# Optimization experiments

Hardware: AMD Instinct MI355X
Metric: run time of the kernel (lower is better)

## Reference

```python
import jax, jax.numpy as jnp
import numpy as np

B, LT, LI, D, H, K = 32, 512, 576, 768, 8, 512


def setup_inputs() -> dict:
    key = jax.random.key(0)
    ks = jax.random.split(key, 10)
    s = 0.02
    return {
        "text_hidden_states": jax.random.normal(ks[0], (B, LT, D), jnp.float32),
        "image_hidden_states": jax.random.normal(ks[1], (B, LI, D), jnp.float32),
        "text_mask": jnp.ones((B, LT), jnp.int32),
        "Wb": jax.random.normal(ks[2], (H, D, D), jnp.float32) * s,   # per-head Linear weights [out,in]
        "Wv": jax.random.normal(ks[3], (K, D), jnp.float32) * s,
        "Wq": jax.random.normal(ks[4], (K, D), jnp.float32) * s,
        "Whv": jax.random.normal(ks[5], (K,), jnp.float32) * s,
        "Whq": jax.random.normal(ks[6], (K,), jnp.float32) * s,
        "Wo": jax.random.normal(ks[7], (D, D * H), jnp.float32) * s,  # output_proj weight [out,in]
        "bo": jnp.zeros((D,), jnp.float32),
    }


def reference(text_hidden_states, image_hidden_states, text_mask, Wb, Wv, Wq, Whv, Whq, Wo, bo):
    text, image = text_hidden_states, image_hidden_states
    # per-head text projection (torch Linear: x @ W.T), batched over heads
    pt = jnp.einsum('bxe,hfe->hbxf', text, Wb)                 # [H,B,LT,D]
    aff = jnp.einsum('hbxe,bye->hbxy', pt, image)              # [H,B,LT,LI]
    wv_v = jnp.einsum('bye,ke->byk', image, Wv)                # [B,LI,K] (head-shared)
    wq_q = jnp.einsum('bxe,ke->bxk', text, Wq)                 # [B,LT,K]
    wqqc = jnp.einsum('bxk,hbxy->hbyk', wq_q, aff)             # [H,B,LI,K]
    wvvc = jnp.einsum('byk,hbxy->hbxk', wv_v, aff)             # [H,B,LT,K]
    h_v = jnp.tanh(wv_v[None] + wqqc)
    h_q = jnp.tanh(wq_q[None] + wvvc)
    att_v = jax.nn.softmax(jnp.einsum('hbyk,k->hby', h_v, Whv), axis=-1)  # over image tokens
    att_q = jax.nn.softmax(jnp.einsum('hbxk,k->hbx', h_q, Whq), axis=-1)  # over text tokens
    ctx_v = jnp.einsum('hby,byd->hbd', att_v, image)
    ctx_q = jnp.einsum('hbx,bxd->hbd', att_q, text)
    head_out = ctx_v + ctx_q                                   # [H,B,D]
    combined = jnp.transpose(head_out, (1, 0, 2)).reshape(text.shape[0], -1)  # [B,H*D]
    return combined @ Wo.T + bo
```

## Files before the change

### kernel.cpp

```cpp
#include <hip/hip_runtime.h>
#include <math.h>

#define B_  32
#define LT_ 512
#define LI_ 576
#define LIP 640
#define D_  768
#define H_  8
#define K_  512
#define NTOK  (LI_ + LT_)
#define CSPLIT 8
#define TPB   (NTOK / CSPLIT)
#define NHEAD ((long)H_ * B_ * D_)

typedef __attribute__((ext_vector_type(4))) short short4v;
typedef __attribute__((ext_vector_type(8))) unsigned short ushort8;
typedef __attribute__((ext_vector_type(8))) _Float16 f16x8;
typedef __attribute__((ext_vector_type(4))) float f32x4;

__device__ __forceinline__ unsigned short f2h(float x) {
  _Float16 h = (_Float16)x;
  return __builtin_bit_cast(unsigned short, h);
}
__device__ __forceinline__ float h2f(unsigned short u) {
  return (float)__builtin_bit_cast(_Float16, u);
}
__device__ __forceinline__ float ftanh(float x) {
  float e = __expf(2.f * x);
  return 1.f - 2.f * __builtin_amdgcn_rcpf(e + 1.f);
}

__device__ __forceinline__ void gl_lds16(const void* g, void* l) {
  __builtin_amdgcn_global_load_lds(
      (const __attribute__((address_space(1))) void*)g,
      (__attribute__((address_space(3))) void*)l, 16, 0, 0);
}

#define EPI_PLAIN 0
#define EPI_T     1
#define EPI_TANH  2
#define EPI_OUT   3

struct Seg {
  const unsigned short *A, *B;
  unsigned short *C, *CT;
  const unsigned short* base;
  const float* wvec;
  float* outv;
  long sA, sB, sC, sCT, sBase;
  int Kd, lda, ldb;
  int gx, gy, nblk, epi, Mlim, valid, ldc, ldt;
};
struct Params { Seg s0, s1, s2; };

__global__ __launch_bounds__(256, 2) void mfma_seg(Params p)
{
  const int orig = blockIdx.x, nwg = gridDim.x;
  const int q8 = nwg >> 3, r8 = nwg & 7;
  const int xcd = orig & 7, idx = orig >> 3;
  const int wg = (xcd < r8 ? xcd * (q8 + 1) : r8 * (q8 + 1) + (xcd - r8) * q8) + idx;

  Seg sg; int local;
  if (wg < p.s0.nblk)                      { sg = p.s0; local = wg; }
  else if (wg < p.s0.nblk + p.s1.nblk)     { sg = p.s1; local = wg - p.s0.nblk; }
  else                                     { sg = p.s2; local = wg - p.s0.nblk - p.s1.nblk; }

  const int bx = local % sg.gx;
  const int tmp2 = local / sg.gx;
  const int by = tmp2 % sg.gy, bz = tmp2 / sg.gy;

  __shared__ unsigned short LDSU[36864];

  const int t = threadIdx.x, lane = t & 63, w = t >> 6;
  const int wr = w >> 1, wc = w & 1;
  const int m0 = bx * 256, n0 = by * 128;
  const int Kd = sg.Kd, lda = sg.lda, ldb = sg.ldb, ldc = sg.ldc;
  const unsigned short* A  = sg.A + (long)bz * sg.sA;
  const unsigned short* Bm = sg.B + (long)bz * sg.sB;

  const int rowb = w * 16 + (lane >> 2);
  const int cswz = ((lane & 3) ^ ((rowb >> 1) & 3)) * 8;
  const bool clampA = (m0 + 256 > sg.Mlim);
  const unsigned short* aSrc = A  + (long)(m0 + rowb) * lda + cswz;
  const unsigned short* bSrc = Bm + (long)(n0 + rowb) * ldb + cswz;
  const int ldsLane = rowb * 32;

  f32x4 acc[8][4];
  #pragma unroll
  for (int i = 0; i < 8; ++i)
    #pragma unroll
    for (int j = 0; j < 4; ++j)
      acc[i][j] = (f32x4){0.f, 0.f, 0.f, 0.f};

  const int rl = lane & 15, g = lane >> 4;
  const int aslot = (g ^ ((rl >> 1) & 3)) << 3;

  auto stage = [&](int bufi, int k0) {
    unsigned short* Ab = LDSU + bufi * 12288;
    unsigned short* Bb = Ab + 8192;
    if (!clampA) {
      #pragma unroll
      for (int q = 0; q < 4; ++q)
        gl_lds16(aSrc + (long)q * 64 * lda + k0, Ab + ldsLane + q * 2048);
    } else {
      #pragma unroll
      for (int q = 0; q < 4; ++q) {
        int rgl = m0 + q * 64 + rowb;
        if (rgl >= sg.Mlim) rgl = sg.Mlim - 1;
        gl_lds16(A + (long)rgl * lda + cswz + k0, Ab + ldsLane + q * 2048);
      }
    }
    #pragma unroll
    for (int q = 0; q < 2; ++q)
      gl_lds16(bSrc + (long)q * 64 * ldb + k0, Bb + ldsLane + q * 2048);
  };

  const int nt = Kd >> 5;
  stage(0, 0);
  if (nt > 1) stage(1, 32);
  if (nt > 2) stage(2, 64);
  int cur = 0;
  for (int tt = 0; tt < nt; ++tt) {
    const int ahead = nt - 1 - tt;
    if (ahead >= 2)      asm volatile("s_waitcnt vmcnt(12)" ::: "memory");
    else if (ahead == 1) asm volatile("s_waitcnt vmcnt(6)"  ::: "memory");
    else                 asm volatile("s_waitcnt vmcnt(0)"  ::: "memory");
    __builtin_amdgcn_s_barrier();
    asm volatile("" ::: "memory");

    const unsigned short* Ab = LDSU + cur * 12288;
    const unsigned short* Bb = Ab + 8192;
    f16x8 af[8], bf[4];
    #pragma unroll
    for (int i = 0; i < 8; ++i)
      af[i] = *(const f16x8*)&Ab[(wr * 128 + i * 16 + rl) * 32 + aslot];
    #pragma unroll
    for (int j = 0; j < 4; ++j)
      bf[j] = *(const f16x8*)&Bb[(wc * 64 + j * 16 + rl) * 32 + aslot];
    __builtin_amdgcn_s_setprio(1);
    #pragma unroll
    for (int i = 0; i < 8; ++i)
      #pragma unroll
      for (int j = 0; j < 4; ++j)
        acc[i][j] = __builtin_amdgcn_mfma_f32_16x16x32_f16(af[i], bf[j], acc[i][j], 0, 0, 0);
    __builtin_amdgcn_s_setprio(0);

    asm volatile("" ::: "memory");
    __builtin_amdgcn_s_barrier();
    if (tt + 3 < nt) stage(cur, (tt + 3) << 5);
    cur = (cur == 2) ? 0 : cur + 1;
  }

  const int rg = lane >> 4;
  if (sg.epi <= EPI_T) {
    unsigned short* C = sg.C + (long)bz * sg.sC;
    #pragma unroll
    for (int i = 0; i < 8; ++i)
      #pragma unroll
      for (int j = 0; j < 4; ++j)
        #pragma unroll
        for (int rr = 0; rr < 4; ++rr) {
          int ml = wr * 128 + i * 16 + rg * 4 + rr;
          int nl = wc * 64 + j * 16 + rl;
          if (m0 + ml < sg.Mlim)
            C[(long)(m0 + ml) * ldc + n0 + nl] = f2h(acc[i][j][rr]);
        }
    if (sg.epi == EPI_T) {
      unsigned short* CT = sg.CT + (long)bz * sg.sCT;
      __syncthreads();
      #pragma unroll
      for (int pp = 0; pp < 2; ++pp) {
        if (wr == pp) {
          #pragma unroll
          for (int i = 0; i < 8; ++i)
            #pragma unroll
            for (int j = 0; j < 4; ++j) {
              int nl = wc * 64 + j * 16 + rl;
              int mh = i * 16 + rg * 4;
              *(short4v*)&LDSU[nl * 136 + mh] = (short4v){
                  (short)f2h(acc[i][j][0]), (short)f2h(acc[i][j][1]),
                  (short)f2h(acc[i][j][2]), (short)f2h(acc[i][j][3])};
            }
        }
        __syncthreads();
        #pragma unroll
        for (int rr = 0; rr < 8; ++rr) {
          int rn = rr * 16 + (t >> 4);
          int m8 = (t & 15) * 8;
          int mg = m0 + pp * 128 + m8;
          if (mg < sg.Mlim)
            *(ushort8*)(CT + (long)(n0 + rn) * sg.ldt + mg) =
                *(const ushort8*)&LDSU[rn * 136 + m8];
        }
        __syncthreads();
      }
    }
  } else if (sg.epi == EPI_TANH) {
    const unsigned short* base = sg.base + (long)bz * sg.sBase;
    float* outp = sg.outv + (long)bz * sg.valid;
    #pragma unroll
    for (int i = 0; i < 8; ++i)
      #pragma unroll
      for (int rr = 0; rr < 4; ++rr) {
        int row = m0 + wr * 128 + i * 16 + rg * 4 + rr;
        if (row < sg.Mlim) {
          float s = 0.f;
          #pragma unroll
          for (int j = 0; j < 4; ++j) {
            int col = n0 + wc * 64 + j * 16 + rl;
            float v = acc[i][j][rr] + h2f(base[(long)row * ldc + col]);
            s += ftanh(v) * sg.wvec[col];
          }
          s += __shfl_xor(s, 1, 64);
          s += __shfl_xor(s, 2, 64);
          s += __shfl_xor(s, 4, 64);
          s += __shfl_xor(s, 8, 64);
          if (rl == 0 && row < sg.valid)
            atomicAdd(&outp[row], s);
        }
      }
  } else {
    float* outp = sg.outv;
    if (wr == 0) {
      #pragma unroll
      for (int i = 0; i < 2; ++i)
        #pragma unroll
        for (int rr = 0; rr < 4; ++rr) {
          int row = i * 16 + rg * 4 + rr;
          #pragma unroll
          for (int j = 0; j < 4; ++j) {
            int col = n0 + wc * 64 + j * 16 + rl;
            atomicAdd(&outp[(long)row * ldc + col], acc[i][j][rr]);
          }
        }
    }
  }
}

struct CSeg { const float* src; unsigned short* dst; long n8; };

__global__ __launch_bounds__(256) void cast_multi(
    CSeg c0, CSeg c1, CSeg c2, CSeg c3, CSeg c4)
{
  long i = (long)blockIdx.x * 256 + threadIdx.x;
  const float* src; unsigned short* dst;
  if      (i < c0.n8)                 { src = c0.src; dst = c0.dst; }
  else if ((i -= c0.n8) < c1.n8)      { src = c1.src; dst = c1.dst; }
  else if ((i -= c1.n8) < c2.n8)      { src = c2.src; dst = c2.dst; }
  else if ((i -= c2.n8) < c3.n8)      { src = c3.src; dst = c3.dst; }
  else if ((i -= c3.n8) < c4.n8)      { src = c4.src; dst = c4.dst; }
  else return;
  float4 v0 = ((const float4*)src)[i * 2];
  float4 v1 = ((const float4*)src)[i * 2 + 1];
  ushort8 o;
  o[0] = f2h(v0.x); o[1] = f2h(v0.y); o[2] = f2h(v0.z); o[3] = f2h(v0.w);
  o[4] = f2h(v1.x); o[5] = f2h(v1.y); o[6] = f2h(v1.z); o[7] = f2h(v1.w);
  *(ushort8*)(dst + i * 8) = o;
}

__global__ __launch_bounds__(256) void cast_pad_image(
    const float* __restrict__ in, unsigned short* __restrict__ out)
{
  long tid = (long)blockIdx.x * 256 + threadIdx.x;
  const long tot = (long)B_ * LIP * (D_ / 8);
  if (tid >= tot) return;
  int e8 = (int)(tid % (D_ / 8));
  long rw = tid / (D_ / 8);
  int y  = (int)(rw % LIP);
  long b = rw / LIP;
  ushort8 o;
  if (y < LI_) {
    const float* p = in + ((b * LI_ + y) * D_ + e8 * 8);
    float4 v0 = *(const float4*)p, v1 = *(const float4*)(p + 4);
    o[0] = f2h(v0.x); o[1] = f2h(v0.y); o[2] = f2h(v0.z); o[3] = f2h(v0.w);
    o[4] = f2h(v1.x); o[5] = f2h(v1.y); o[6] = f2h(v1.z); o[7] = f2h(v1.w);
  } else {
    #pragma unroll
    for (int j = 0; j < 8; ++j) o[j] = 0;
  }
  *(ushort8*)(out + rw * D_ + e8 * 8) = o;
}

__global__ __launch_bounds__(256) void zero_f32(float* __restrict__ p, long n) {
  long i = (long)blockIdx.x * 256 + threadIdx.x;
  if (i < n) p[i] = 0.f;
}

__global__ __launch_bounds__(256) void init_out(
    const float* __restrict__ bo, float* __restrict__ out)
{
  int i = blockIdx.x * 256 + threadIdx.x;
  out[i] = bo[i % D_];
}

__global__ __launch_bounds__(256) void softmax_att(
    const float* __restrict__ lv, const float* __restrict__ lq,
    float* __restrict__ attvG, float* __restrict__ attqG)
{
  const int b = blockIdx.x, h = blockIdx.y;
  const int t = threadIdx.x;
  __shared__ float buf[LI_];
  __shared__ float red[4];

  const float* lvp = lv + ((long)h * B_ + b) * LI_;
  float m = -1e30f;
  for (int i = t; i < LI_; i += 256) m = fmaxf(m, lvp[i]);
  #pragma unroll
  for (int o = 32; o > 0; o >>= 1) m = fmaxf(m, __shfl_down(m, o, 64));
  if ((t & 63) == 0) red[t >> 6] = m;
  __syncthreads();
  m = fmaxf(fmaxf(red[0], red[1]), fmaxf(red[2], red[3]));
  __syncthreads();
  float s = 0.f;
  for (int i = t; i < LI_; i += 256) { float e = __expf(lvp[i] - m); buf[i] = e; s += e; }
  #pragma unroll
  for (int o = 32; o > 0; o >>= 1) s += __shfl_down(s, o, 64);
  if ((t & 63) == 0) red[t >> 6] = s;
  __syncthreads();
  s = red[0] + red[1] + red[2] + red[3];
  {
    float inv = 1.f / s;
    float* op = attvG + ((long)h * B_ + b) * LI_;
    for (int i = t; i < LI_; i += 256) op[i] = buf[i] * inv;
  }
  __syncthreads();

  const float* lqp = lq + ((long)h * B_ + b) * LT_;
  m = -1e30f;
  for (int i = t; i < LT_; i += 256) m = fmaxf(m, lqp[i]);
  #pragma unroll
  for (int o = 32; o > 0; o >>= 1) m = fmaxf(m, __shfl_down(m, o, 64));
  if ((t & 63) == 0) red[t >> 6] = m;
  __syncthreads();
  m = fmaxf(fmaxf(red[0], red[1]), fmaxf(red[2], red[3]));
  __syncthreads();
  s = 0.f;
  for (int i = t; i < LT_; i += 256) { float e = __expf(lqp[i] - m); buf[i] = e; s += e; }
  #pragma unroll
  for (int o = 32; o > 0; o >>= 1) s += __shfl_down(s, o, 64);
  if ((t & 63) == 0) red[t >> 6] = s;
  __syncthreads();
  s = red[0] + red[1] + red[2] + red[3];
  {
    float inv = 1.f / s;
    float* op = attqG + ((long)h * B_ + b) * LT_;
    for (int i = t; i < LT_; i += 256) op[i] = buf[i] * inv;
  }
}

__global__ __launch_bounds__(256) void ctx_part(
    const float* __restrict__ attvG, const float* __restrict__ attqG,
    const unsigned short* __restrict__ text_h,
    float* __restrict__ head_part)
{
  const int b = blockIdx.x, d0 = blockIdx.y * 128, s = blockIdx.z;
  const int t = threadIdx.x, dl = t & 127, g = t >> 7;
  const long IMG_OFF = (long)B_ * LT_ * D_;
  __shared__ float wts[H_][TPB];
  __shared__ long  roff[TPB];
  __shared__ float red[H_][128];
  const int tok0 = s * TPB;
  for (int i = t; i < H_ * TPB; i += 256) {
    int h = i / TPB, j = i % TPB, tok = tok0 + j;
    wts[h][j] = tok < LI_ ? attvG[((long)h * B_ + b) * LI_ + tok]
                          : attqG[((long)h * B_ + b) * LT_ + (tok - LI_)];
  }
  if (t < TPB) {
    int tok = tok0 + t;
    roff[t] = tok < LI_ ? IMG_OFF + ((long)b * LIP + tok) * D_
                        : ((long)b * LT_ + (tok - LI_)) * D_;
  }
  __syncthreads();
  float acc[H_];
  #pragma unroll
  for (int h = 0; h < H_; ++h) acc[h] = 0.f;
  #pragma unroll 4
  for (int j = g; j < TPB; j += 2) {
    float val = h2f(text_h[roff[j] + d0 + dl]);
    #pragma unroll
    for (int h = 0; h < H_; ++h) acc[h] = fmaf(wts[h][j], val, acc[h]);
  }
  if (g == 1) {
    #pragma unroll
    for (int h = 0; h < H_; ++h) red[h][dl] = acc[h];
  }
  __syncthreads();
  if (g == 0) {
    float* hp = head_part + (long)s * NHEAD;
    #pragma unroll
    for (int h = 0; h < H_; ++h)
      hp[((long)h * B_ + b) * D_ + d0 + dl] = acc[h] + red[h][dl];
  }
}

__global__ __launch_bounds__(256) void reduce_head(
    const float* __restrict__ head_part, unsigned short* __restrict__ head16)
{
  long i = (long)blockIdx.x * 256 + threadIdx.x;
  float s = 0.f;
  #pragma unroll
  for (int p = 0; p < CSPLIT; ++p) s += head_part[(long)p * NHEAD + i];
  int d = (int)(i % D_);
  long hb = i / D_;
  int b = (int)(hb % B_), h = (int)(hb / B_);
  head16[(long)b * (H_ * D_) + (long)h * D_ + d] = f2h(s);
}

extern "C" void kernel_launch(void* const* d_in, const int* in_sizes, int n_in,
                              void* d_out, int out_size, void* d_ws, size_t ws_size,
                              hipStream_t stream)
{
  const float* text  = (const float*)d_in[0];
  const float* image = (const float*)d_in[1];
  const float* Wb  = (const float*)d_in[3];
  const float* Wv  = (const float*)d_in[4];
  const float* Wq  = (const float*)d_in[5];
  const float* Whv = (const float*)d_in[6];
  const float* Whq = (const float*)d_in[7];
  const float* Wo  = (const float*)d_in[8];
  const float* bo  = (const float*)d_in[9];
  float* out = (float*)d_out;

  const long N_TEXT = (long)B_ * LT_ * D_;
  const long N_IMGP = (long)B_ * LIP * D_;
  const long N_WV   = (long)K_ * D_;
  const long N_WB   = (long)H_ * D_ * D_;
  const long N_WO   = (long)D_ * H_ * D_;
  const long N_WVV  = (long)B_ * LIP * K_;
  const long N_WQQ  = (long)B_ * LT_ * K_;
  const long N_PT   = (long)B_ * LT_ * D_;
  const long N_AFF  = (long)B_ * LT_ * LIP;
  const long N_LV   = (long)H_ * B_ * LI_;
  const long N_LQ   = (long)H_ * B_ * LT_;
  const long N_H16  = (long)B_ * H_ * D_;

  unsigned short* wsu = (unsigned short*)d_ws;
  long off = 0;
  unsigned short* text_h  = wsu + off; off += N_TEXT;
  unsigned short* image_p = wsu + off; off += N_IMGP;
  unsigned short* Wv_h    = wsu + off; off += N_WV;
  unsigned short* Wq_h    = wsu + off; off += N_WV;
  unsigned short* Wb_h    = wsu + off; off += N_WB;
  unsigned short* Wo_h    = wsu + off; off += N_WO;
  unsigned short* wv_v    = wsu + off; off += N_WVV;
  unsigned short* wq_q    = wsu + off; off += N_WQQ;
  unsigned short* wv_vT   = wsu + off; off += N_WVV;
  unsigned short* wq_qT   = wsu + off; off += N_WQQ;
  unsigned short* pt_h    = wsu + off; off += N_PT;
  unsigned short* aff     = wsu + off; off += N_AFF;
  unsigned short* affT    = wsu + off; off += N_AFF;
  unsigned short* head16  = wsu + off; off += N_H16;
  float* lv        = (float*)(wsu + off);
  float* lq        = lv + N_LV;
  float* attvG     = lq + N_LQ;
  float* attqG     = attvG + N_LV;
  float* head_part = attqG + N_LQ;
  const size_t need = (size_t)off * 2 +
      (size_t)(2 * (N_LV + N_LQ) + CSPLIT * NHEAD) * 4;
  if (ws_size < need) return;

  dim3 blk(256);

  {
    CSeg c0{text, text_h, N_TEXT / 8};
    CSeg c1{Wv,   Wv_h,   N_WV / 8};
    CSeg c2{Wq,   Wq_h,   N_WV / 8};
    CSeg c3{Wb,   Wb_h,   N_WB / 8};
    CSeg c4{Wo,   Wo_h,   N_WO / 8};
    long tot8 = c0.n8 + c1.n8 + c2.n8 + c3.n8 + c4.n8;
    cast_multi<<<(unsigned)((tot8 + 255) / 256), blk, 0, stream>>>(c0, c1, c2, c3, c4);
  }
  cast_pad_image<<<(unsigned)((B_ * LIP * (D_ / 8) + 255) / 256), blk, 0, stream>>>(image, image_p);
  zero_f32<<<(unsigned)((N_LV + N_LQ + 255) / 256), blk, 0, stream>>>(lv, N_LV + N_LQ);
  init_out<<<(unsigned)(B_ * D_ / 256), blk, 0, stream>>>(bo, out);

  Seg zs{};  zs.nblk = 0;

  {
    Seg s0{}; s0.A = image_p; s0.B = Wv_h; s0.C = wv_v; s0.CT = wv_vT;
    s0.sA = (long)LIP * D_; s0.sC = (long)LIP * K_; s0.sCT = (long)K_ * LIP;
    s0.Kd = D_; s0.lda = D_; s0.ldb = D_;
    s0.gx = 3; s0.gy = 4; s0.nblk = 3 * 4 * B_; s0.epi = EPI_T;
    s0.Mlim = LIP; s0.ldc = K_; s0.ldt = LIP;

    Seg s1{}; s1.A = text_h; s1.B = Wq_h; s1.C = wq_q; s1.CT = wq_qT;
    s1.sA = (long)LT_ * D_; s1.sC = (long)LT_ * K_; s1.sCT = (long)K_ * LT_;
    s1.Kd = D_; s1.lda = D_; s1.ldb = D_;
    s1.gx = 2; s1.gy = 4; s1.nblk = 2 * 4 * B_; s1.epi = EPI_T;
    s1.Mlim = LT_; s1.ldc = K_; s1.ldt = LT_;

    Seg s2{}; s2.A = text_h; s2.B = Wb_h; s2.C = pt_h;
    s2.Kd = D_; s2.lda = D_; s2.ldb = D_;
    s2.gx = 64; s2.gy = 6; s2.nblk = 64 * 6; s2.epi = EPI_PLAIN;
    s2.Mlim = B_ * LT_; s2.ldc = D_;

    Params P{s0, s1, s2};
    mfma_seg<<<s0.nblk + s1.nblk + s2.nblk, blk, 0, stream>>>(P);
  }

  for (int h = 0; h < H_; ++h) {
    {
      Seg s0{}; s0.A = pt_h; s0.B = image_p; s0.C = aff; s0.CT = affT;
      s0.sA = (long)LT_ * D_; s0.sB = (long)LIP * D_;
      s0.sC = (long)LT_ * LIP; s0.sCT = (long)LIP * LT_;
      s0.Kd = D_; s0.lda = D_; s0.ldb = D_;
      s0.gx = 2; s0.gy = 5; s0.nblk = 2 * 5 * B_; s0.epi = EPI_T;
      s0.Mlim = LT_; s0.ldc = LIP; s0.ldt = LT_;
      Params P{s0, zs, zs};
      mfma_seg<<<s0.nblk, blk, 0, stream>>>(P);
    }
    {
      Seg s0{}; s0.A = affT; s0.B = wq_qT;
      s0.base = wv_v; s0.wvec = Whv; s0.outv = lv + (long)h * B_ * LI_;
      s0.sA = (long)LIP * LT_; s0.sB = (long)K_ * LT_; s0.sBase = (long)LIP * K_;
      s0.Kd = LT_; s0.lda = LT_; s0.ldb = LT_;
      s0.gx = 3; s0.gy = 4; s0.nblk = 3 * 4 * B_; s0.epi = EPI_TANH;
      s0.Mlim = LIP; s0.valid = LI_; s0.ldc = K_;

      Seg s1{}; s1.A = aff; s1.B = wv_vT;
      s1.base = wq_q; s1.wvec = Whq; s1.outv = lq + (long)h * B_ * LT_;
      s1.sA = (long)LT_ * LIP; s1.sB = (long)K_ * LIP; s1.sBase = (long)LT_ * K_;
      s1.Kd = LIP; s1.lda = LIP; s1.ldb = LIP;
      s1.gx = 2; s1.gy = 4; s1.nblk = 2 * 4 * B_; s1.epi = EPI_TANH;
      s1.Mlim = LT_; s1.valid = LT_; s1.ldc = K_;

      Seg s2 = zs;
      if (h < H_ - 1) {
        s2.A = text_h; s2.B = Wb_h + (long)(h + 1) * D_ * D_; s2.C = pt_h;
        s2.Kd = D_; s2.lda = D_; s2.ldb = D_;
        s2.gx = 64; s2.gy = 6; s2.nblk = 64 * 6; s2.epi = EPI_PLAIN;
        s2.Mlim = B_ * LT_; s2.ldc = D_;
      }
      Params P{s0, s1, s2};
      mfma_seg<<<s0.nblk + s1.nblk + s2.nblk, blk, 0, stream>>>(P);
    }
  }

  softmax_att<<<dim3(B_, H_), blk, 0, stream>>>(lv, lq, attvG, attqG);
  ctx_part<<<dim3(B_, D_ / 128, CSPLIT), blk, 0, stream>>>(attvG, attqG, text_h, head_part);
  reduce_head<<<(unsigned)(NHEAD / 256), blk, 0, stream>>>(head_part, head16);

  {
    Seg s0{}; s0.A = head16; s0.B = Wo_h; s0.outv = out;
    s0.sA = (long)(H_ * D_ / 8); s0.sB = (long)(H_ * D_ / 8);
    s0.Kd = H_ * D_ / 8; s0.lda = H_ * D_; s0.ldb = H_ * D_;
    s0.gx = 1; s0.gy = 6; s0.nblk = 1 * 6 * 8; s0.epi = EPI_OUT;
    s0.Mlim = B_; s0.valid = B_; s0.ldc = D_;
    Params P{s0, zs, zs};
    mfma_seg<<<s0.nblk, blk, 0, stream>>>(P);
  }
}
```

Before: 1.068 ms.

## Shrink MFMA GEMM tile to 128x128 for higher occupancy and more blocks

Cuts the per-block M tile from 256 to 128 rows, which reduces accumulator registers and LDS. Launch bounds rise to three blocks per CU and the grid sizes are doubled to match. LDS fragment loads now use explicit ds_read_b128 with a waitcnt and a sched barrier ahead of the MFMAs. The transpose epilogue is simplified into a single pass. In exchange, each block reuses less data per K step, so more global and LDS traffic is needed per flop.

```diff
diff --git a/kernel.cpp b/kernel.cpp
--- a/kernel.cpp
+++ b/kernel.cpp
@@ -36,6 +36,14 @@
       (__attribute__((address_space(3))) void*)l, 16, 0, 0);
 }
 
+__device__ __forceinline__ f16x8 lds_read16(const unsigned short* p) {
+  f16x8 r;
+  const __attribute__((address_space(3))) unsigned short* lp =
+      (const __attribute__((address_space(3))) unsigned short*)p;
+  asm volatile("ds_read_b128 %0, %1" : "=v"(r) : "v"(lp));
+  return r;
+}
+
 #define EPI_PLAIN 0
 #define EPI_T     1
 #define EPI_TANH  2
@@ -53,7 +61,7 @@
 };
 struct Params { Seg s0, s1, s2; };
 
-__global__ __launch_bounds__(256, 2) void mfma_seg(Params p)
+__global__ __launch_bounds__(256, 3) void mfma_seg(Params p)
 {
   const int orig = blockIdx.x, nwg = gridDim.x;
   const int q8 = nwg >> 3, r8 = nwg & 7;
@@ -69,25 +77,25 @@
   const int tmp2 = local / sg.gx;
   const int by = tmp2 % sg.gy, bz = tmp2 / sg.gy;
 
-  __shared__ unsigned short LDSU[36864];
+  __shared__ unsigned short LDSU[24576];
 
   const int t = threadIdx.x, lane = t & 63, w = t >> 6;
   const int wr = w >> 1, wc = w & 1;
-  const int m0 = bx * 256, n0 = by * 128;
+  const int m0 = bx * 128, n0 = by * 128;
   const int Kd = sg.Kd, lda = sg.lda, ldb = sg.ldb, ldc = sg.ldc;
   const unsigned short* A  = sg.A + (long)bz * sg.sA;
   const unsigned short* Bm = sg.B + (long)bz * sg.sB;
 
-  const int rowb = w * 16 + (lane >> 2);
-  const int cswz = ((lane & 3) ^ ((rowb >> 1) & 3)) * 8;
-  const bool clampA = (m0 + 256 > sg.Mlim);
-  const unsigned short* aSrc = A  + (long)(m0 + rowb) * lda + cswz;
-  const unsigned short* bSrc = Bm + (long)(n0 + rowb) * ldb + cswz;
-  const int ldsLane = rowb * 32;
-
-  f32x4 acc[8][4];
-  #pragma unroll
-  for (int i = 0; i < 8; ++i)
+  const int srow = w * 16 + (lane >> 2);
+  const int cswz = ((lane & 3) ^ ((srow >> 1) & 3)) * 8;
+  const bool clampA = (m0 + 128 > sg.Mlim);
+  const unsigned short* aSrc = A  + (long)(m0 + srow) * lda + cswz;
+  const unsigned short* bSrc = Bm + (long)(n0 + srow) * ldb + cswz;
+  const int ldsLane = w * 512 + lane * 8;
+
+  f32x4 acc[4][4];
+  #pragma unroll
+  for (int i = 0; i < 4; ++i)
     #pragma unroll
     for (int j = 0; j < 4; ++j)
       acc[i][j] = (f32x4){0.f, 0.f, 0.f, 0.f};
@@ -96,23 +104,20 @@
   const int aslot = (g ^ ((rl >> 1) & 3)) << 3;
 
   auto stage = [&](int bufi, int k0) {
-    unsigned short* Ab = LDSU + bufi * 12288;
-    unsigned short* Bb = Ab + 8192;
+    unsigned short* Ab = LDSU + bufi * 8192;
+    unsigned short* Bb = Ab + 4096;
     if (!clampA) {
-      #pragma unroll
-      for (int q = 0; q < 4; ++q)
-        gl_lds16(aSrc + (long)q * 64 * lda + k0, Ab + ldsLane + q * 2048);
+      gl_lds16(aSrc + k0,                 Ab + ldsLane);
+      gl_lds16(aSrc + (long)64 * lda + k0, Ab + ldsLane + 2048);
     } else {
-      #pragma unroll
-      for (int q = 0; q < 4; ++q) {
-        int rgl = m0 + q * 64 + rowb;
-        if (rgl >= sg.Mlim) rgl = sg.Mlim - 1;
-        gl_lds16(A + (long)rgl * lda + cswz + k0, Ab + ldsLane + q * 2048);
-      }
+      int r0 = m0 + srow, r1 = r0 + 64;
+      if (r0 >= sg.Mlim) r0 = sg.Mlim - 1;
+      if (r1 >= sg.Mlim) r1 = sg.Mlim - 1;
+      gl_lds16(A + (long)r0 * lda + cswz + k0, Ab + ldsLane);
+      gl_lds16(A + (long)r1 * lda + cswz + k0, Ab + ldsLane + 2048);
     }
-    #pragma unroll
-    for (int q = 0; q < 2; ++q)
-      gl_lds16(bSrc + (long)q * 64 * ldb + k0, Bb + ldsLane + q * 2048);
+    gl_lds16(bSrc + k0,                 Bb + ldsLane);
+    gl_lds16(bSrc + (long)64 * ldb + k0, Bb + ldsLane + 2048);
   };
 
   const int nt = Kd >> 5;
@@ -122,30 +127,31 @@
   int cur = 0;
   for (int tt = 0; tt < nt; ++tt) {
     const int ahead = nt - 1 - tt;
-    if (ahead >= 2)      asm volatile("s_waitcnt vmcnt(12)" ::: "memory");
-    else if (ahead == 1) asm volatile("s_waitcnt vmcnt(6)"  ::: "memory");
-    else                 asm volatile("s_waitcnt vmcnt(0)"  ::: "memory");
+    if (ahead >= 2)      asm volatile("s_waitcnt vmcnt(8)" ::: "memory");
+    else if (ahead == 1) asm volatile("s_waitcnt vmcnt(4)" ::: "memory");
+    else                 asm volatile("s_waitcnt vmcnt(0)" ::: "memory");
     __builtin_amdgcn_s_barrier();
-    asm volatile("" ::: "memory");
-
-    const unsigned short* Ab = LDSU + cur * 12288;
-    const unsigned short* Bb = Ab + 8192;
-    f16x8 af[8], bf[4];
-    #pragma unroll
-    for (int i = 0; i < 8; ++i)
-      af[i] = *(const f16x8*)&Ab[(wr * 128 + i * 16 + rl) * 32 + aslot];
+
+    const unsigned short* Ab = LDSU + cur * 8192;
+    const unsigned short* Bb = Ab + 4096;
+    f16x8 af[4], bf[4];
+    #pragma unroll
+    for (int i = 0; i < 4; ++i)
+      af[i] = lds_read16(&Ab[(wr * 64 + i * 16 + rl) * 32 + aslot]);
     #pragma unroll
     for (int j = 0; j < 4; ++j)
-      bf[j] = *(const f16x8*)&Bb[(wc * 64 + j * 16 + rl) * 32 + aslot];
+      bf[j] = lds_read16(&Bb[(wc * 64 + j * 16 + rl) * 32 + aslot]);
+    asm volatile("s_waitcnt lgkmcnt(0)" ::: "memory");
+    __builtin_amdgcn_sched_barrier(0);
+
     __builtin_amdgcn_s_setprio(1);
     #pragma unroll
-    for (int i = 0; i < 8; ++i)
+    for (int i = 0; i < 4; ++i)
       #pragma unroll
       for (int j = 0; j < 4; ++j)
         acc[i][j] = __builtin_amdgcn_mfma_f32_16x16x32_f16(af[i], bf[j], acc[i][j], 0, 0, 0);
     __builtin_amdgcn_s_setprio(0);
 
-    asm volatile("" ::: "memory");
     __builtin_amdgcn_s_barrier();
     if (tt + 3 < nt) stage(cur, (tt + 3) << 5);
     cur = (cur == 2) ? 0 : cur + 1;
@@ -154,55 +160,49 @@
   const int rg = lane >> 4;
   if (sg.epi <= EPI_T) {
     unsigned short* C = sg.C + (long)bz * sg.sC;
-    #pragma unroll
-    for (int i = 0; i < 8; ++i)
+    unsigned short hv[4][4][4];
+    #pragma unroll
+    for (int i = 0; i < 4; ++i)
       #pragma unroll
       for (int j = 0; j < 4; ++j)
         #pragma unroll
         for (int rr = 0; rr < 4; ++rr) {
-          int ml = wr * 128 + i * 16 + rg * 4 + rr;
+          int ml = wr * 64 + i * 16 + rg * 4 + rr;
           int nl = wc * 64 + j * 16 + rl;
+          hv[i][j][rr] = f2h(acc[i][j][rr]);
           if (m0 + ml < sg.Mlim)
-            C[(long)(m0 + ml) * ldc + n0 + nl] = f2h(acc[i][j][rr]);
+            C[(long)(m0 + ml) * ldc + n0 + nl] = hv[i][j][rr];
         }
     if (sg.epi == EPI_T) {
       unsigned short* CT = sg.CT + (long)bz * sg.sCT;
+      #pragma unroll
+      for (int i = 0; i < 4; ++i)
+        #pragma unroll
+        for (int j = 0; j < 4; ++j) {
+          int nl = wc * 64 + j * 16 + rl;
+          int mh = wr * 64 + i * 16 + rg * 4;
+          *(short4v*)&LDSU[nl * 136 + mh] = (short4v){
+              (short)hv[i][j][0], (short)hv[i][j][1],
+              (short)hv[i][j][2], (short)hv[i][j][3]};
+        }
       __syncthreads();
       #pragma unroll
-      for (int pp = 0; pp < 2; ++pp) {
-        if (wr == pp) {
-          #pragma unroll
-          for (int i = 0; i < 8; ++i)
-            #pragma unroll
-            for (int j = 0; j < 4; ++j) {
-              int nl = wc * 64 + j * 16 + rl;
-              int mh = i * 16 + rg * 4;
-              *(short4v*)&LDSU[nl * 136 + mh] = (short4v){
-                  (short)f2h(acc[i][j][0]), (short)f2h(acc[i][j][1]),
-                  (short)f2h(acc[i][j][2]), (short)f2h(acc[i][j][3])};
-            }
-        }
-        __syncthreads();
-        #pragma unroll
-        for (int rr = 0; rr < 8; ++rr) {
-          int rn = rr * 16 + (t >> 4);
-          int m8 = (t & 15) * 8;
-          int mg = m0 + pp * 128 + m8;
-          if (mg < sg.Mlim)
-            *(ushort8*)(CT + (long)(n0 + rn) * sg.ldt + mg) =
-                *(const ushort8*)&LDSU[rn * 136 + m8];
-        }
-        __syncthreads();
+      for (int rr = 0; rr < 8; ++rr) {
+        int rn = rr * 16 + (t >> 4);
+        int m8 = (t & 15) * 8;
+        if (m0 + m8 < sg.Mlim)
+          *(ushort8*)(CT + (long)(n0 + rn) * sg.ldt + m0 + m8) =
+              *(const ushort8*)&LDSU[rn * 136 + m8];
       }
     }
   } else if (sg.epi == EPI_TANH) {
     const unsigned short* base = sg.base + (long)bz * sg.sBase;
     float* outp = sg.outv + (long)bz * sg.valid;
     #pragma unroll
-    for (int i = 0; i < 8; ++i)
+    for (int i = 0; i < 4; ++i)
       #pragma unroll
       for (int rr = 0; rr < 4; ++rr) {
-        int row = m0 + wr * 128 + i * 16 + rg * 4 + rr;
+        int row = m0 + wr * 64 + i * 16 + rg * 4 + rr;
         if (row < sg.Mlim) {
           float s = 0.f;
           #pragma unroll
@@ -480,18 +480,18 @@
     Seg s0{}; s0.A = image_p; s0.B = Wv_h; s0.C = wv_v; s0.CT = wv_vT;
     s0.sA = (long)LIP * D_; s0.sC = (long)LIP * K_; s0.sCT = (long)K_ * LIP;
     s0.Kd = D_; s0.lda = D_; s0.ldb = D_;
-    s0.gx = 3; s0.gy = 4; s0.nblk = 3 * 4 * B_; s0.epi = EPI_T;
+    s0.gx = 5; s0.gy = 4; s0.nblk = 5 * 4 * B_; s0.epi = EPI_T;
     s0.Mlim = LIP; s0.ldc = K_; s0.ldt = LIP;
 
     Seg s1{}; s1.A = text_h; s1.B = Wq_h; s1.C = wq_q; s1.CT = wq_qT;
     s1.sA = (long)LT_ * D_; s1.sC = (long)LT_ * K_; s1.sCT = (long)K_ * LT_;
     s1.Kd = D_; s1.lda = D_; s1.ldb = D_;
-    s1.gx = 2; s1.gy = 4; s1.nblk = 2 * 4 * B_; s1.epi = EPI_T;
+    s1.gx = 4; s1.gy = 4; s1.nblk = 4 * 4 * B_; s1.epi = EPI_T;
     s1.Mlim = LT_; s1.ldc = K_; s1.ldt = LT_;
 
     Seg s2{}; s2.A = text_h; s2.B = Wb_h; s2.C = pt_h;
     s2.Kd = D_; s2.lda = D_; s2.ldb = D_;
-    s2.gx = 64; s2.gy = 6; s2.nblk = 64 * 6; s2.epi = EPI_PLAIN;
+    s2.gx = 128; s2.gy = 6; s2.nblk = 128 * 6; s2.epi = EPI_PLAIN;
     s2.Mlim = B_ * LT_; s2.ldc = D_;
 
     Params P{s0, s1, s2};
@@ -504,7 +504,7 @@
       s0.sA = (long)LT_ * D_; s0.sB = (long)LIP * D_;
       s0.sC = (long)LT_ * LIP; s0.sCT = (long)LIP * LT_;
       s0.Kd = D_; s0.lda = D_; s0.ldb = D_;
-      s0.gx = 2; s0.gy = 5; s0.nblk = 2 * 5 * B_; s0.epi = EPI_T;
+      s0.gx = 4; s0.gy = 5; s0.nblk = 4 * 5 * B_; s0.epi = EPI_T;
       s0.Mlim = LT_; s0.ldc = LIP; s0.ldt = LT_;
       Params P{s0, zs, zs};
       mfma_seg<<<s0.nblk, blk, 0, stream>>>(P);
@@ -514,21 +514,21 @@
       s0.base = wv_v; s0.wvec = Whv; s0.outv = lv + (long)h * B_ * LI_;
       s0.sA = (long)LIP * LT_; s0.sB = (long)K_ * LT_; s0.sBase = (long)LIP * K_;
       s0.Kd = LT_; s0.lda = LT_; s0.ldb = LT_;
-      s0.gx = 3; s0.gy = 4; s0.nblk = 3 * 4 * B_; s0.epi = EPI_TANH;
+      s0.gx = 5; s0.gy = 4; s0.nblk = 5 * 4 * B_; s0.epi = EPI_TANH;
       s0.Mlim = LIP; s0.valid = LI_; s0.ldc = K_;
 
       Seg s1{}; s1.A = aff; s1.B = wv_vT;
       s1.base = wq_q; s1.wvec = Whq; s1.outv = lq + (long)h * B_ * LT_;
       s1.sA = (long)LT_ * LIP; s1.sB = (long)K_ * LIP; s1.sBase = (long)LT_ * K_;
       s1.Kd = LIP; s1.lda = LIP; s1.ldb = LIP;
-      s1.gx = 2; s1.gy = 4; s1.nblk = 2 * 4 * B_; s1.epi = EPI_TANH;
+      s1.gx = 4; s1.gy = 4; s1.nblk = 4 * 4 * B_; s1.epi = EPI_TANH;
       s1.Mlim = LT_; s1.valid = LT_; s1.ldc = K_;
 
       Seg s2 = zs;
       if (h < H_ - 1) {
         s2.A = text_h; s2.B = Wb_h + (long)(h + 1) * D_ * D_; s2.C = pt_h;
         s2.Kd = D_; s2.lda = D_; s2.ldb = D_;
-        s2.gx = 64; s2.gy = 6; s2.nblk = 64 * 6; s2.epi = EPI_PLAIN;
+        s2.gx = 128; s2.gy = 6; s2.nblk = 128 * 6; s2.epi = EPI_PLAIN;
         s2.Mlim = B_ * LT_; s2.ldc = D_;
       }
       Params P{s0, s1, s2};
```

New measurement: 972.2 us. -8.9%, faster.
